# Kernel optimization log

Hardware: AMD Instinct MI355X
Metric: run time of the kernel (lower is better)

## Reference

```python
import jax, jax.numpy as jnp
import numpy as np

LRELU_SLOPE = 0.01  # torch nn.LeakyReLU default


def _lrelu(v):
    return jnp.where(v > 0, v, LRELU_SLOPE * v)


def setup_inputs() -> dict:
    key = jax.random.key(0)
    ks = jax.random.split(key, 9)
    B, C, T = 16, 1024, 1500
    nbins, hid, emb = 4096, 512, 256
    s = 0.02
    return {
        "feature": jax.random.normal(ks[0], (B, C, T), jnp.float32),
        "centroid": jax.random.normal(ks[1], (nbins, C), jnp.float32),
        "ew0": jax.random.normal(ks[2], (hid, C), jnp.float32) * s,
        "eb0": jnp.zeros((hid,), jnp.float32),
        "ew1": jax.random.normal(ks[3], (hid, hid), jnp.float32) * s,
        "eb1": jnp.zeros((hid,), jnp.float32),
        "ew2": jax.random.normal(ks[4], (emb, hid), jnp.float32) * s,
        "eb2": jnp.zeros((emb,), jnp.float32),
        "dw0": jax.random.normal(ks[5], (hid, emb), jnp.float32) * s,
        "db0": jnp.zeros((hid,), jnp.float32),
        "dw1": jax.random.normal(ks[6], (hid, hid), jnp.float32) * s,
        "db1": jnp.zeros((hid,), jnp.float32),
        "dw2": jax.random.normal(ks[7], (C, hid), jnp.float32) * s,
        "db2": jnp.zeros((C,), jnp.float32),
    }


def reference(feature, centroid, ew0, eb0, ew1, eb1, ew2, eb2,
              dw0, db0, dw1, db1, dw2, db2):
    B, C, T = feature.shape
    # --- nearest-centroid match: squared-norm expansion + matmul + argmin ---
    x = feature.transpose(0, 2, 1).reshape(-1, C)          # (B*T, C)
    c_norm = jnp.sum(centroid * centroid, axis=1)          # (nbins,)
    dist = (jnp.sum(x * x, axis=1, keepdims=True)
            - 2.0 * (x @ centroid.T)
            + c_norm[None, :])                             # (B*T, nbins)
    idx = jnp.argmin(dist, axis=1)                         # (B*T,)
    lin_dec = centroid[idx].reshape(B, T, C).transpose(0, 2, 1)  # (B, C, T)
    # --- speaker residual + refiner autoencoder (quantizer = identity) ---
    spk_raw = feature - lin_dec                            # (B, C, T)
    h = spk_raw.transpose(0, 2, 1)                         # (B, T, C)
    h = _lrelu(h @ ew0.T + eb0)
    h = _lrelu(h @ ew1.T + eb1)
    z = h @ ew2.T + eb2                                    # (B, T, emb)
    h = _lrelu(z @ dw0.T + db0)
    h = _lrelu(h @ dw1.T + db1)
    spk_dec = (h @ dw2.T + db2).transpose(0, 2, 1)         # (B, C, T)
    return lin_dec + spk_dec
```

## Files before the change

kernel.cpp:

```cpp
#include <hip/hip_runtime.h>


typedef unsigned short u16;
typedef unsigned int   u32;
typedef __bf16 bf16x8 __attribute__((ext_vector_type(8)));
typedef float  f32x4  __attribute__((ext_vector_type(4)));

#define AS1 __attribute__((address_space(1)))
#define AS3 __attribute__((address_space(3)))

__device__ __forceinline__ u16 rne_bf16(float f) {
  u32 u = __float_as_uint(f);
  u = (u + 0x7FFFu + ((u >> 16) & 1u)) >> 16;
  return (u16)u;
}
__device__ __forceinline__ float b2f(u16 h) {
  return __uint_as_float(((u32)h) << 16);
}


__global__ __launch_bounds__(256) void conv_centroid(
    const float* __restrict__ cent, u16* __restrict__ chi, u16* __restrict__ clo,
    float* __restrict__ cnorm, int K)
{
  int row  = blockIdx.x * 4 + (threadIdx.x >> 6);
  int lane = threadIdx.x & 63;
  const float* cr = cent + (size_t)row * K;
  float s = 0.f;
  for (int j = 0; j < K; j += 64) {
    int k = j + lane;
    float f = cr[k];
    s += f * f;
    u32 u = __float_as_uint(f);
    u32 hi = (u + 0x7FFFu + ((u >> 16) & 1u)) >> 16;
    float fhi = __uint_as_float(hi << 16);
    chi[(size_t)row * K + k] = (u16)hi;
    clo[(size_t)row * K + k] = rne_bf16(f - fhi);
  }
#pragma unroll
  for (int m = 1; m < 64; m <<= 1) s += __shfl_xor(s, m, 64);
  if (lane == 0) cnorm[row] = s;
}

__global__ __launch_bounds__(256) void conv_feature(
    const float* __restrict__ feat, u16* __restrict__ xhi, u16* __restrict__ xlo,
    int C, int T)
{
  __shared__ float tile[64][65];
  int bb = blockIdx.z, c0 = blockIdx.y * 64, t0 = blockIdx.x * 64;
  const float* fb = feat + (size_t)bb * C * T;
#pragma unroll
  for (int i = 0; i < 16; ++i) {
    int id = threadIdx.x + i * 256;
    int lc = id >> 6, lt = id & 63;
    int t = t0 + lt;
    tile[lc][lt] = (t < T) ? fb[(size_t)(c0 + lc) * T + t] : 0.f;
  }
  __syncthreads();
#pragma unroll
  for (int i = 0; i < 16; ++i) {
    int id = threadIdx.x + i * 256;
    int lt = id >> 6, lc = id & 63;
    int t = t0 + lt;
    if (t < T) {
      size_t row = (size_t)bb * T + t;
      float f = tile[lc][lt];
      u32 u = __float_as_uint(f);
      u32 hi = (u + 0x7FFFu + ((u >> 16) & 1u)) >> 16;
      float fhi = __uint_as_float(hi << 16);
      xhi[row * C + c0 + lc] = (u16)hi;
      xlo[row * C + c0 + lc] = rne_bf16(f - fhi);
    }
  }
}

__global__ __launch_bounds__(256) void f2bf(
    const float* __restrict__ s, u16* __restrict__ d, int n)
{
  int i = blockIdx.x * 256 + threadIdx.x;
  if (i < n) d[i] = rne_bf16(s[i]);
}


template<int KK, int NSEG>
__global__ __launch_bounds__(512, 2) void score256(
    const u16* __restrict__ A0, const u16* __restrict__ A1, const u16* __restrict__ A2,
    const u16* __restrict__ B0s, const u16* __restrict__ B1s, const u16* __restrict__ B2s,
    const float* __restrict__ cnb, float* __restrict__ pval, int* __restrict__ pidx,
    int M, int N)
{
  constexpr int NKTPS = KK / 64;
  constexpr int NKT   = NSEG * NKTPS;
  static_assert(NKT % 2 == 0, "even tile count");

  __shared__ f32x4 smem4[8192];
  char* smem = (char*)smem4;

  const int lane = threadIdx.x & 63;
  const int wid  = threadIdx.x >> 6;
  const int wr   = wid >> 2;
  const int wc   = wid & 3;

  const int rowBase = blockIdx.y * 256;
  const int colBase = blockIdx.x * 256;

  const int kswz  = ((lane & 7) ^ (lane >> 3)) << 4;
  const int kbase = (lane >> 4) << 4;

  const f32x4 zero4 = {0.f, 0.f, 0.f, 0.f};
  f32x4 acc[8][4];
#pragma unroll
  for (int i = 0; i < 8; ++i)
#pragma unroll
    for (int j = 0; j < 4; ++j) acc[i][j] = zero4;

  bf16x8 aR[4][2];
  bf16x8 bR[2][2][2];

  auto stageA = [&](int b, int h, int t) {
    int tc  = t < NKT ? t : NKT - 1;
    int seg = tc / NKTPS;
    int k0  = (tc - seg * NKTPS) << 6;
    const u16* S = (seg == 0 ? A0 : (seg == 1 ? A1 : A2));
    char* dst = smem + b * 32768 + h * 16384 + wid * 1024;
#pragma unroll
    for (int j = 0; j < 2; ++j) {
      int r  = h * 128 + j * 64 + wid * 8 + (lane >> 3);
      int gr = rowBase + r; gr = gr < M ? gr : M - 1;
      const char* ga = (const char*)S + ((size_t)gr * KK + k0) * 2 + kswz;
      __builtin_amdgcn_global_load_lds((const AS1 void*)ga,
                                       (AS3 void*)(dst + j * 8192), 16, 0, 0);
    }
  };
  auto stageB = [&](int b, int h, int t) {
    int tc  = t < NKT ? t : NKT - 1;
    int seg = tc / NKTPS;
    int k0  = (tc - seg * NKTPS) << 6;
    const u16* S = (seg == 0 ? B0s : (seg == 1 ? B1s : B2s));
    char* dst = smem + 65536 + b * 32768 + h * 16384 + wid * 1024;
#pragma unroll
    for (int j = 0; j < 2; ++j) {
      int r  = h * 128 + j * 64 + wid * 8 + (lane >> 3);
      int gr = colBase + r;
      const char* ga = (const char*)S + ((size_t)gr * KK + k0) * 2 + kswz;
      __builtin_amdgcn_global_load_lds((const AS1 void*)ga,
                                       (AS3 void*)(dst + j * 8192), 16, 0, 0);
    }
  };

#define LDA_Q(b, qm) do { \
  _Pragma("unroll") for (int mf = 0; mf < 4; ++mf) { \
    int row = wr * 128 + (qm) * 64 + mf * 16 + (lane & 15); \
    const char* p = smem + (b) * 32768 + row * 128; \
    int sw = (row & 7) << 4; \
    aR[mf][0] = *(const bf16x8*)(p + (kbase ^ sw)); \
    aR[mf][1] = *(const bf16x8*)(p + ((kbase + 64) ^ sw)); \
  } } while (0)

#define LDB_Q(b, qn) do { \
  _Pragma("unroll") for (int nf = 0; nf < 2; ++nf) { \
    int row = wc * 64 + (qn) * 32 + nf * 16 + (lane & 15); \
    const char* p = smem + 65536 + (b) * 32768 + row * 128; \
    int sw = (row & 7) << 4; \
    bR[qn][nf][0] = *(const bf16x8*)(p + (kbase ^ sw)); \
    bR[qn][nf][1] = *(const bf16x8*)(p + ((kbase + 64) ^ sw)); \
  } } while (0)

#define MMQ(qm, qn) do { \
  _Pragma("unroll") for (int mf = 0; mf < 4; ++mf) \
  _Pragma("unroll") for (int nf = 0; nf < 2; ++nf) { \
    acc[(qm)*4+mf][(qn)*2+nf] = __builtin_amdgcn_mfma_f32_16x16x32_bf16( \
        aR[mf][0], bR[qn][nf][0], acc[(qm)*4+mf][(qn)*2+nf], 0, 0, 0); \
    acc[(qm)*4+mf][(qn)*2+nf] = __builtin_amdgcn_mfma_f32_16x16x32_bf16( \
        aR[mf][1], bR[qn][nf][1], acc[(qm)*4+mf][(qn)*2+nf], 0, 0, 0); \
  } } while (0)

#define BAR()     __builtin_amdgcn_s_barrier()
#define PRIO1()   __builtin_amdgcn_s_setprio(1)
#define PRIO0()   __builtin_amdgcn_s_setprio(0)
#define VMCNT4()  asm volatile("s_waitcnt vmcnt(4)" ::: "memory")
#define LGKM8()   asm volatile("s_waitcnt lgkmcnt(8)" ::: "memory")
#define LGKM0_SB() do { asm volatile("s_waitcnt lgkmcnt(0)" ::: "memory"); \
                        __builtin_amdgcn_sched_barrier(0); } while (0)

  stageA(0, 0, 0); stageA(0, 1, 0); stageB(0, 0, 0); stageB(0, 1, 0);
  stageB(1, 0, 1); stageB(1, 1, 1);
  VMCNT4();
  BAR();

  for (int i = 0; i < NKT / 2; ++i) {
    const int t = 2 * i;
    LDA_Q(0, 0); LDB_Q(0, 0);
    stageA(1, 0, t + 1);
    LGKM8();
    BAR(); LGKM0_SB(); PRIO1(); MMQ(0, 0); PRIO0(); BAR();
    LDB_Q(0, 1);
    stageA(1, 1, t + 1);
    BAR(); LGKM0_SB(); PRIO1(); MMQ(0, 1); PRIO0(); BAR();
    LDA_Q(0, 1);
    stageB(0, 0, t + 2);
    BAR(); LGKM0_SB(); PRIO1(); MMQ(1, 1); PRIO0(); BAR();
    stageB(0, 1, t + 2);
    VMCNT4();
    BAR(); PRIO1(); MMQ(1, 0); PRIO0(); BAR();
    LDA_Q(1, 0); LDB_Q(1, 0);
    stageA(0, 0, t + 2);
    LGKM8();
    BAR(); LGKM0_SB(); PRIO1(); MMQ(0, 0); PRIO0(); BAR();
    LDB_Q(1, 1);
    stageA(0, 1, t + 2);
    BAR(); LGKM0_SB(); PRIO1(); MMQ(0, 1); PRIO0(); BAR();
    LDA_Q(1, 1);
    stageB(1, 0, t + 3);
    BAR(); LGKM0_SB(); PRIO1(); MMQ(1, 1); PRIO0(); BAR();
    stageB(1, 1, t + 3);
    VMCNT4();
    BAR(); PRIO1(); MMQ(1, 0); PRIO0(); BAR();
  }

  const int colL = colBase + wc * 64 + (lane & 15);
  float cn[4];
#pragma unroll
  for (int ni = 0; ni < 4; ++ni) cn[ni] = 0.5f * cnb[colL + ni * 16];
  const int nchunk = N >> 6;
  const int chunk  = (colBase >> 6) + wc;
#pragma unroll
  for (int mi = 0; mi < 8; ++mi) {
#pragma unroll
    for (int reg = 0; reg < 4; ++reg) {
      float best = acc[mi][0][reg] - cn[0];
      int   bc   = colL;
#pragma unroll
      for (int ni = 1; ni < 4; ++ni) {
        float v  = acc[mi][ni][reg] - cn[ni];
        int   c2 = colL + ni * 16;
        if (v > best || (v == best && c2 < bc)) { best = v; bc = c2; }
      }
#pragma unroll
      for (int m = 1; m < 16; m <<= 1) {
        float vo = __shfl_xor(best, m, 64);
        int   co = __shfl_xor(bc,   m, 64);
        if (vo > best || (vo == best && co < bc)) { best = vo; bc = co; }
      }
      if ((lane & 15) == 0) {
        int row = rowBase + wr * 128 + (mi >> 2) * 64 + (mi & 3) * 16
                + ((lane >> 4) << 2) + reg;
        if (row < M) {
          pval[(size_t)row * nchunk + chunk] = best;
          pidx[(size_t)row * nchunk + chunk] = bc;
        }
      }
    }
  }
#undef LDA_Q
#undef LDB_Q
#undef MMQ
#undef BAR
#undef PRIO1
#undef PRIO0
#undef VMCNT4
#undef LGKM8
#undef LGKM0_SB
}


template<int NSEG, bool SCORE, bool ACT>
__global__ __launch_bounds__(256) void gemm_bt(
    const u16* __restrict__ A0, const u16* __restrict__ A1, const u16* __restrict__ A2,
    const u16* __restrict__ B0, const u16* __restrict__ B1, const u16* __restrict__ B2,
    const float* __restrict__ cnb, u16* __restrict__ outb,
    float* __restrict__ pval, int* __restrict__ pidx,
    int M, int N, int K)
{
  __shared__ bf16x8 smem8[2048];
  char* smem = (char*)smem8;

  const int lane = threadIdx.x & 63;
  const int wid  = threadIdx.x >> 6;
  const int wm   = wid >> 1, wn = wid & 1;

  const int rowBase = blockIdx.y * 128;
  const int colBase = blockIdx.x * 128;

  const f32x4 zero4 = {0.f, 0.f, 0.f, 0.f};
  f32x4 acc[4][4];
#pragma unroll
  for (int i = 0; i < 4; ++i)
#pragma unroll
    for (int j = 0; j < 4; ++j) acc[i][j] = zero4;

  const int l8   = lane >> 3;
  const int kbsw = ((lane & 7) ^ l8) << 4;
  const int kseg = K >> 6;
  const int nkt  = NSEG * kseg;

  for (int kt = 0; kt < nkt; ++kt) {
    int seg, k0;
    if (NSEG == 1) { seg = 0; k0 = kt << 6; }
    else           { seg = kt / kseg; k0 = (kt - seg * kseg) << 6; }
    const u16* Aseg = (seg == 0) ? A0 : (seg == 1 ? A1 : A2);
    const u16* Bseg = (seg == 0) ? B0 : (seg == 1 ? B1 : B2);

#pragma unroll
    for (int i = 0; i < 4; ++i) {
      int c = wid * 4 + i;
      int r = c * 8 + l8;
      int gra = rowBase + r; gra = gra < M ? gra : (M - 1);
      const char* ga = (const char*)Aseg + ((size_t)gra * K + k0) * 2 + kbsw;
      __builtin_amdgcn_global_load_lds((const AS1 void*)ga,
                                       (AS3 void*)(smem + c * 1024), 16, 0, 0);
      int grb = colBase + r;
      const char* gb = (const char*)Bseg + ((size_t)grb * K + k0) * 2 + kbsw;
      __builtin_amdgcn_global_load_lds((const AS1 void*)gb,
                                       (AS3 void*)(smem + 16384 + c * 1024), 16, 0, 0);
    }
    __syncthreads();

#pragma unroll
    for (int kk = 0; kk < 64; kk += 32) {
      bf16x8 a[4], b[4];
      const int kb = (kk + ((lane >> 4) << 3)) << 1;
#pragma unroll
      for (int mf = 0; mf < 4; ++mf) {
        int row = wm * 64 + mf * 16 + (lane & 15);
        a[mf] = *(const bf16x8*)(smem + row * 128 + (kb ^ ((row & 7) << 4)));
      }
#pragma unroll
      for (int nf = 0; nf < 4; ++nf) {
        int row = wn * 64 + nf * 16 + (lane & 15);
        b[nf] = *(const bf16x8*)(smem + 16384 + row * 128 + (kb ^ ((row & 7) << 4)));
      }
#pragma unroll
      for (int mf = 0; mf < 4; ++mf)
#pragma unroll
        for (int nf = 0; nf < 4; ++nf)
          acc[mf][nf] = __builtin_amdgcn_mfma_f32_16x16x32_bf16(
              a[mf], b[nf], acc[mf][nf], 0, 0, 0);
    }
    __syncthreads();
  }

  const int colLane = colBase + wn * 64 + (lane & 15);

  if (SCORE) {
    float cn[4];
#pragma unroll
    for (int nf = 0; nf < 4; ++nf) cn[nf] = 0.5f * cnb[colLane + nf * 16];
    const int nchunk = N >> 6;
    const int chunk  = (colBase >> 6) + wn;
#pragma unroll
    for (int mf = 0; mf < 4; ++mf) {
#pragma unroll
      for (int reg = 0; reg < 4; ++reg) {
        float best = acc[mf][0][reg] - cn[0];
        int   bc   = colLane;
#pragma unroll
        for (int nf = 1; nf < 4; ++nf) {
          float v = acc[mf][nf][reg] - cn[nf];
          int c2 = colLane + nf * 16;
          if (v > best || (v == best && c2 < bc)) { best = v; bc = c2; }
        }
#pragma unroll
        for (int m = 1; m < 16; m <<= 1) {
          float vo = __shfl_xor(best, m, 64);
          int   co = __shfl_xor(bc,   m, 64);
          if (vo > best || (vo == best && co < bc)) { best = vo; bc = co; }
        }
        if ((lane & 15) == 0) {
          int row = rowBase + wm * 64 + mf * 16 + ((lane >> 4) << 2) + reg;
          if (row < M) {
            pval[(size_t)row * nchunk + chunk] = best;
            pidx[(size_t)row * nchunk + chunk] = bc;
          }
        }
      }
    }
  } else {
    float bl[4];
#pragma unroll
    for (int nf = 0; nf < 4; ++nf) bl[nf] = cnb[colLane + nf * 16];
#pragma unroll
    for (int mf = 0; mf < 4; ++mf)
#pragma unroll
      for (int nf = 0; nf < 4; ++nf)
#pragma unroll
        for (int reg = 0; reg < 4; ++reg) {
          int row = rowBase + wm * 64 + mf * 16 + ((lane >> 4) << 2) + reg;
          if (row < M) {
            float v = acc[mf][nf][reg] + bl[nf];
            if (ACT) v = v > 0.f ? v : 0.01f * v;
            outb[(size_t)row * N + colLane + nf * 16] = rne_bf16(v);
          }
        }
  }
}


__global__ __launch_bounds__(256) void argmax_reduce(
    const float* __restrict__ pval, const int* __restrict__ pidx,
    int* __restrict__ idxOut, int nchunk)
{
  int row  = blockIdx.x * 4 + (threadIdx.x >> 6);
  int lane = threadIdx.x & 63;
  float v = pval[(size_t)row * nchunk + lane];
  int   c = pidx[(size_t)row * nchunk + lane];
#pragma unroll
  for (int m = 1; m < 64; m <<= 1) {
    float vo = __shfl_xor(v, m, 64);
    int   co = __shfl_xor(c, m, 64);
    if (vo > v || (vo == v && co < c)) { v = vo; c = co; }
  }
  if (lane == 0) idxOut[row] = c;
}

__global__ __launch_bounds__(256) void build_spk(
    const u16* __restrict__ xhi, const u16* __restrict__ xlo,
    const float* __restrict__ cent, const int* __restrict__ idx,
    u16* __restrict__ spk, int C)
{
  int row = blockIdx.x;
  const float* cr = cent + (size_t)idx[row] * C;
  size_t base = (size_t)row * C;
  for (int c = threadIdx.x; c < C; c += 256) {
    float v = b2f(xhi[base + c]) + b2f(xlo[base + c]) - cr[c];
    spk[base + c] = rne_bf16(v);
  }
}

__global__ __launch_bounds__(256) void transpose_out(
    const u16* __restrict__ spkdec, const float* __restrict__ cent,
    const int* __restrict__ idx, float* __restrict__ out, int C, int T)
{
  __shared__ float tile[64][65];
  int r0 = blockIdx.x * 64, c0 = blockIdx.y * 64;
#pragma unroll
  for (int i = 0; i < 16; ++i) {
    int id = threadIdx.x + i * 256;
    int lr = id >> 6, lc = id & 63;
    int row = r0 + lr;
    tile[lr][lc] = b2f(spkdec[(size_t)row * C + c0 + lc])
                 + cent[(size_t)idx[row] * C + c0 + lc];
  }
  __syncthreads();
#pragma unroll
  for (int i = 0; i < 16; ++i) {
    int id = threadIdx.x + i * 256;
    int lc = id >> 6, lr = id & 63;
    int row = r0 + lr;
    int b = row / T, t = row - b * T;
    out[((size_t)b * C + c0 + lc) * T + t] = tile[lr][lc];
  }
}


extern "C" void kernel_launch(void* const* d_in, const int* in_sizes, int n_in,
                              void* d_out, int out_size, void* d_ws, size_t ws_size,
                              hipStream_t stream)
{
  const float* feature  = (const float*)d_in[0];
  const float* centroid = (const float*)d_in[1];
  const float* ew0 = (const float*)d_in[2];
  const float* eb0 = (const float*)d_in[3];
  const float* ew1 = (const float*)d_in[4];
  const float* eb1 = (const float*)d_in[5];
  const float* ew2 = (const float*)d_in[6];
  const float* eb2 = (const float*)d_in[7];
  const float* dw0 = (const float*)d_in[8];
  const float* db0 = (const float*)d_in[9];
  const float* dw1 = (const float*)d_in[10];
  const float* db1 = (const float*)d_in[11];
  const float* dw2 = (const float*)d_in[12];
  const float* db2 = (const float*)d_in[13];
  float* out = (float*)d_out;

  const int Bb = 16, C = 1024, T = 1500, M = Bb * T;
  const int NBIN = 4096, HID = 512, EMB = 256;
  const int MB  = (M + 127) / 128;
  const int MB2 = (M + 255) / 256;

  char* ws = (char*)d_ws;
  size_t off = 0;
  auto alloc = [&](size_t bytes) -> char* {
    char* p = ws + off;
    off += (bytes + 255) & ~(size_t)255;
    return p;
  };
  u16*   c_hi  = (u16*)  alloc((size_t)NBIN * C * 2);
  u16*   c_lo  = (u16*)  alloc((size_t)NBIN * C * 2);
  float* cnorm = (float*)alloc((size_t)NBIN * 4);
  u16*   wb0   = (u16*)  alloc((size_t)HID * C   * 2);
  u16*   wb1   = (u16*)  alloc((size_t)HID * HID * 2);
  u16*   wb2   = (u16*)  alloc((size_t)EMB * HID * 2);
  u16*   wb3   = (u16*)  alloc((size_t)HID * EMB * 2);
  u16*   wb4   = (u16*)  alloc((size_t)HID * HID * 2);
  u16*   wb5   = (u16*)  alloc((size_t)C   * HID * 2);
  u16*   x_hi  = (u16*)  alloc((size_t)M * C * 2);
  u16*   x_lo  = (u16*)  alloc((size_t)M * C * 2);
  int*   idx   = (int*)  alloc((size_t)M * 4);
  char*  spkR  =         alloc((size_t)M * C * 2);
  u16*   spk   = (u16*)spkR;
  float* pval  = (float*)spkR;
  int*   pidx  = (int*)(spkR + (size_t)M * 64 * 4);
  u16*   h1    = (u16*)  alloc((size_t)M * HID * 2);
  u16*   h2    = (u16*)  alloc((size_t)M * HID * 2);
  u16*   hz    = (u16*)  alloc((size_t)M * EMB * 2);

  conv_centroid<<<NBIN / 4, 256, 0, stream>>>(centroid, c_hi, c_lo, cnorm, C);
  conv_feature<<<dim3((T + 63) / 64, C / 64, Bb), 256, 0, stream>>>(feature, x_hi, x_lo, C, T);
  f2bf<<<(HID * C   + 255) / 256, 256, 0, stream>>>(ew0, wb0, HID * C);
  f2bf<<<(HID * HID + 255) / 256, 256, 0, stream>>>(ew1, wb1, HID * HID);
  f2bf<<<(EMB * HID + 255) / 256, 256, 0, stream>>>(ew2, wb2, EMB * HID);
  f2bf<<<(HID * EMB + 255) / 256, 256, 0, stream>>>(dw0, wb3, HID * EMB);
  f2bf<<<(HID * HID + 255) / 256, 256, 0, stream>>>(dw1, wb4, HID * HID);
  f2bf<<<(C   * HID + 255) / 256, 256, 0, stream>>>(dw2, wb5, C * HID);

  score256<1024, 3><<<dim3(NBIN / 256, MB2), 512, 0, stream>>>(
      x_hi, x_lo, x_hi, c_hi, c_hi, c_lo, cnorm, pval, pidx, M, NBIN);

  argmax_reduce<<<M / 4, 256, 0, stream>>>(pval, pidx, idx, NBIN / 64);
  build_spk<<<M, 256, 0, stream>>>(x_hi, x_lo, centroid, idx, spk, C);

  gemm_bt<1, false, true ><<<dim3(HID / 128, MB), 256, 0, stream>>>(
      spk, spk, spk, wb0, wb0, wb0, eb0, h1, nullptr, nullptr, M, HID, C);
  gemm_bt<1, false, true ><<<dim3(HID / 128, MB), 256, 0, stream>>>(
      h1, h1, h1, wb1, wb1, wb1, eb1, h2, nullptr, nullptr, M, HID, HID);
  gemm_bt<1, false, false><<<dim3(EMB / 128, MB), 256, 0, stream>>>(
      h2, h2, h2, wb2, wb2, wb2, eb2, hz, nullptr, nullptr, M, EMB, HID);
  gemm_bt<1, false, true ><<<dim3(HID / 128, MB), 256, 0, stream>>>(
      hz, hz, hz, wb3, wb3, wb3, db0, h1, nullptr, nullptr, M, HID, EMB);
  gemm_bt<1, false, true ><<<dim3(HID / 128, MB), 256, 0, stream>>>(
      h1, h1, h1, wb4, wb4, wb4, db1, h2, nullptr, nullptr, M, HID, HID);
  gemm_bt<1, false, false><<<dim3(C / 128, MB), 256, 0, stream>>>(
      h2, h2, h2, wb5, wb5, wb5, db2, spk, nullptr, nullptr, M, C, HID);

  transpose_out<<<dim3(M / 64, C / 64), 256, 0, stream>>>(spk, centroid, idx, out, C, T);
}
```

Before: 1.016 ms.

## Replace three-pass split-bf16 centroid scoring with bf16 pass plus candidate rescan

```diff
diff --git a/kernel.cpp b/kernel.cpp
--- a/kernel.cpp
+++ b/kernel.cpp
@@ -8,6 +8,8 @@
 
 #define AS1 __attribute__((address_space(1)))
 #define AS3 __attribute__((address_space(3)))
+
+#define LIST_CAP 2048
 
 __device__ __forceinline__ u16 rne_bf16(float f) {
   u32 u = __float_as_uint(f);
@@ -264,61 +266,88 @@
 }
 
 
-template<int NSEG, bool SCORE, bool ACT>
-__global__ __launch_bounds__(256) void gemm_bt(
-    const u16* __restrict__ A0, const u16* __restrict__ A1, const u16* __restrict__ A2,
-    const u16* __restrict__ B0, const u16* __restrict__ B1, const u16* __restrict__ B2,
-    const float* __restrict__ cnb, u16* __restrict__ outb,
-    float* __restrict__ pval, int* __restrict__ pidx,
-    int M, int N, int K)
-{
-  __shared__ bf16x8 smem8[2048];
-  char* smem = (char*)smem8;
-
-  const int lane = threadIdx.x & 63;
-  const int wid  = threadIdx.x >> 6;
+__global__ __launch_bounds__(256) void cand_select(
+    const float* __restrict__ pval1, int* __restrict__ lists,
+    int* __restrict__ cnt)
+{
+  int row  = blockIdx.x * 4 + (threadIdx.x >> 6);
+  int lane = threadIdx.x & 63;
+  float v = pval1[(size_t)row * 64 + lane];
+  float m = v;
+#pragma unroll
+  for (int s = 1; s < 64; s <<= 1) m = fmaxf(m, __shfl_xor(m, s, 64));
+  if (v >= m - 1.0f) {
+    int pos = atomicAdd(&cnt[lane], 1);
+    if (pos < LIST_CAP) lists[lane * LIST_CAP + pos] = row;
+  }
+}
+
+
+template<int KK>
+__global__ __launch_bounds__(256) void rescan(
+    const u16* __restrict__ xhi, const u16* __restrict__ xlo,
+    const u16* __restrict__ chi, const u16* __restrict__ clo,
+    const float* __restrict__ cnorm,
+    const int* __restrict__ lists, const int* __restrict__ cnt,
+    float* __restrict__ pval2, int* __restrict__ pidx2)
+{
+  __shared__ char  smem[24576];
+  __shared__ int   rlist[128];
+  __shared__ float sval[128];
+  __shared__ int   sidx[128];
+
+  const int chunk = blockIdx.x;
+  const int n     = cnt[chunk];
+  const int m0    = blockIdx.y * 128;
+  if (m0 >= n) return;
+
+  const int tid  = threadIdx.x;
+  const int lane = tid & 63;
+  const int wid  = tid >> 6;
   const int wm   = wid >> 1, wn = wid & 1;
 
-  const int rowBase = blockIdx.y * 128;
-  const int colBase = blockIdx.x * 128;
+  if (tid < 128) {
+    int m = m0 + tid;
+    rlist[tid] = lists[chunk * LIST_CAP + (m < n ? m : n - 1)];
+  }
+  __syncthreads();
+
+  const int kswz = ((lane & 7) ^ (lane >> 3)) << 4;
+  size_t aoff[4];
+#pragma unroll
+  for (int j = 0; j < 4; ++j) {
+    int r = (wid * 4 + j) * 8 + (lane >> 3);
+    aoff[j] = (size_t)rlist[r] * KK * 2 + kswz;
+  }
+  size_t boff[2];
+#pragma unroll
+  for (int j = 0; j < 2; ++j) {
+    int r = (wid * 2 + j) * 8 + (lane >> 3);
+    boff[j] = (size_t)(chunk * 64 + r) * KK * 2 + kswz;
+  }
 
   const f32x4 zero4 = {0.f, 0.f, 0.f, 0.f};
-  f32x4 acc[4][4];
-#pragma unroll
-  for (int i = 0; i < 4; ++i)
-#pragma unroll
-    for (int j = 0; j < 4; ++j) acc[i][j] = zero4;
-
-  const int l8   = lane >> 3;
-  const int kbsw = ((lane & 7) ^ l8) << 4;
-  const int kseg = K >> 6;
-  const int nkt  = NSEG * kseg;
-
-  for (int kt = 0; kt < nkt; ++kt) {
-    int seg, k0;
-    if (NSEG == 1) { seg = 0; k0 = kt << 6; }
-    else           { seg = kt / kseg; k0 = (kt - seg * kseg) << 6; }
-    const u16* Aseg = (seg == 0) ? A0 : (seg == 1 ? A1 : A2);
-    const u16* Bseg = (seg == 0) ? B0 : (seg == 1 ? B1 : B2);
-
-#pragma unroll
-    for (int i = 0; i < 4; ++i) {
-      int c = wid * 4 + i;
-      int r = c * 8 + l8;
-      int gra = rowBase + r; gra = gra < M ? gra : (M - 1);
-      const char* ga = (const char*)Aseg + ((size_t)gra * K + k0) * 2 + kbsw;
-      __builtin_amdgcn_global_load_lds((const AS1 void*)ga,
-                                       (AS3 void*)(smem + c * 1024), 16, 0, 0);
-      int grb = colBase + r;
-      const char* gb = (const char*)Bseg + ((size_t)grb * K + k0) * 2 + kbsw;
-      __builtin_amdgcn_global_load_lds((const AS1 void*)gb,
-                                       (AS3 void*)(smem + 16384 + c * 1024), 16, 0, 0);
-    }
+  f32x4 acc[4][2];
+#pragma unroll
+  for (int i = 0; i < 4; ++i) { acc[i][0] = zero4; acc[i][1] = zero4; }
+
+  for (int kt = 0; kt < 3 * (KK / 64); ++kt) {
+    int seg = kt / (KK / 64);
+    int k0b = (kt % (KK / 64)) << 7;
+    const char* Asrc = (const char*)(seg == 1 ? xlo : xhi) + k0b;
+    const char* Bsrc = (const char*)(seg == 2 ? clo : chi) + k0b;
+#pragma unroll
+    for (int j = 0; j < 4; ++j)
+      __builtin_amdgcn_global_load_lds((const AS1 void*)(Asrc + aoff[j]),
+          (AS3 void*)(smem + (wid * 4 + j) * 1024), 16, 0, 0);
+#pragma unroll
+    for (int j = 0; j < 2; ++j)
+      __builtin_amdgcn_global_load_lds((const AS1 void*)(Bsrc + boff[j]),
+          (AS3 void*)(smem + 16384 + (wid * 2 + j) * 1024), 16, 0, 0);
     __syncthreads();
-
 #pragma unroll
     for (int kk = 0; kk < 64; kk += 32) {
-      bf16x8 a[4], b[4];
+      bf16x8 a[4], b[2];
       const int kb = (kk + ((lane >> 4) << 3)) << 1;
 #pragma unroll
       for (int mf = 0; mf < 4; ++mf) {
@@ -326,72 +355,63 @@
         a[mf] = *(const bf16x8*)(smem + row * 128 + (kb ^ ((row & 7) << 4)));
       }
 #pragma unroll
-      for (int nf = 0; nf < 4; ++nf) {
-        int row = wn * 64 + nf * 16 + (lane & 15);
+      for (int nf = 0; nf < 2; ++nf) {
+        int row = wn * 32 + nf * 16 + (lane & 15);
         b[nf] = *(const bf16x8*)(smem + 16384 + row * 128 + (kb ^ ((row & 7) << 4)));
       }
 #pragma unroll
       for (int mf = 0; mf < 4; ++mf)
 #pragma unroll
-        for (int nf = 0; nf < 4; ++nf)
+        for (int nf = 0; nf < 2; ++nf)
           acc[mf][nf] = __builtin_amdgcn_mfma_f32_16x16x32_bf16(
               a[mf], b[nf], acc[mf][nf], 0, 0, 0);
     }
     __syncthreads();
   }
 
-  const int colLane = colBase + wn * 64 + (lane & 15);
-
-  if (SCORE) {
-    float cn[4];
-#pragma unroll
-    for (int nf = 0; nf < 4; ++nf) cn[nf] = 0.5f * cnb[colLane + nf * 16];
-    const int nchunk = N >> 6;
-    const int chunk  = (colBase >> 6) + wn;
-#pragma unroll
-    for (int mf = 0; mf < 4; ++mf) {
+  const int colL = chunk * 64 + wn * 32 + (lane & 15);
+  const float cn0 = 0.5f * cnorm[colL];
+  const float cn1 = 0.5f * cnorm[colL + 16];
+  float rbest[4][4]; int rbc[4][4];
+#pragma unroll
+  for (int mf = 0; mf < 4; ++mf)
+#pragma unroll
+    for (int reg = 0; reg < 4; ++reg) {
+      float best = acc[mf][0][reg] - cn0;
+      int   bc   = colL;
+      float v1   = acc[mf][1][reg] - cn1;
+      if (v1 > best || (v1 == best && colL + 16 < bc)) { best = v1; bc = colL + 16; }
+#pragma unroll
+      for (int m = 1; m < 16; m <<= 1) {
+        float vo = __shfl_xor(best, m, 64);
+        int   co = __shfl_xor(bc,   m, 64);
+        if (vo > best || (vo == best && co < bc)) { best = vo; bc = co; }
+      }
+      rbest[mf][reg] = best; rbc[mf][reg] = bc;
+    }
+  if (wn == 1 && (lane & 15) == 0) {
+#pragma unroll
+    for (int mf = 0; mf < 4; ++mf)
 #pragma unroll
       for (int reg = 0; reg < 4; ++reg) {
-        float best = acc[mf][0][reg] - cn[0];
-        int   bc   = colLane;
-#pragma unroll
-        for (int nf = 1; nf < 4; ++nf) {
-          float v = acc[mf][nf][reg] - cn[nf];
-          int c2 = colLane + nf * 16;
-          if (v > best || (v == best && c2 < bc)) { best = v; bc = c2; }
-        }
-#pragma unroll
-        for (int m = 1; m < 16; m <<= 1) {
-          float vo = __shfl_xor(best, m, 64);
-          int   co = __shfl_xor(bc,   m, 64);
-          if (vo > best || (vo == best && co < bc)) { best = vo; bc = co; }
-        }
-        if ((lane & 15) == 0) {
-          int row = rowBase + wm * 64 + mf * 16 + ((lane >> 4) << 2) + reg;
-          if (row < M) {
-            pval[(size_t)row * nchunk + chunk] = best;
-            pidx[(size_t)row * nchunk + chunk] = bc;
-          }
-        }
-      }
-    }
-  } else {
-    float bl[4];
-#pragma unroll
-    for (int nf = 0; nf < 4; ++nf) bl[nf] = cnb[colLane + nf * 16];
+        int rloc = wm * 64 + mf * 16 + ((lane >> 4) << 2) + reg;
+        sval[rloc] = rbest[mf][reg]; sidx[rloc] = rbc[mf][reg];
+      }
+  }
+  __syncthreads();
+  if (wn == 0 && (lane & 15) == 0) {
 #pragma unroll
     for (int mf = 0; mf < 4; ++mf)
 #pragma unroll
-      for (int nf = 0; nf < 4; ++nf)
-#pragma unroll
-        for (int reg = 0; reg < 4; ++reg) {
-          int row = rowBase + wm * 64 + mf * 16 + ((lane >> 4) << 2) + reg;
-          if (row < M) {
-            float v = acc[mf][nf][reg] + bl[nf];
-            if (ACT) v = v > 0.f ? v : 0.01f * v;
-            outb[(size_t)row * N + colLane + nf * 16] = rne_bf16(v);
-          }
-        }
+      for (int reg = 0; reg < 4; ++reg) {
+        int rloc = wm * 64 + mf * 16 + ((lane >> 4) << 2) + reg;
+        float best = rbest[mf][reg]; int bc = rbc[mf][reg];
+        float vo = sval[rloc]; int co = sidx[rloc];
+        if (vo > best || (vo == best && co < bc)) { best = vo; bc = co; }
+        int row = rlist[rloc];
+        pval2[(size_t)row * 64 + chunk] = best;
+        pidx2[(size_t)row * 64 + chunk] = bc;
+      }
   }
 }
 
@@ -450,6 +470,95 @@
     int b = row / T, t = row - b * T;
     out[((size_t)b * C + c0 + lc) * T + t] = tile[lr][lc];
   }
+}
+
+
+template<int NSEG, bool ACT>
+__global__ __launch_bounds__(256) void gemm_bt(
+    const u16* __restrict__ A0,
+    const u16* __restrict__ B0,
+    const float* __restrict__ cnb, u16* __restrict__ outb,
+    int M, int N, int K)
+{
+  __shared__ bf16x8 smem8[2048];
+  char* smem = (char*)smem8;
+
+  const int lane = threadIdx.x & 63;
+  const int wid  = threadIdx.x >> 6;
+  const int wm   = wid >> 1, wn = wid & 1;
+
+  const int rowBase = blockIdx.y * 128;
+  const int colBase = blockIdx.x * 128;
+
+  const f32x4 zero4 = {0.f, 0.f, 0.f, 0.f};
+  f32x4 acc[4][4];
+#pragma unroll
+  for (int i = 0; i < 4; ++i)
+#pragma unroll
+    for (int j = 0; j < 4; ++j) acc[i][j] = zero4;
+
+  const int l8   = lane >> 3;
+  const int kbsw = ((lane & 7) ^ l8) << 4;
+  const int nkt  = K >> 6;
+
+  for (int kt = 0; kt < nkt; ++kt) {
+    int k0 = kt << 6;
+#pragma unroll
+    for (int i = 0; i < 4; ++i) {
+      int c = wid * 4 + i;
+      int r = c * 8 + l8;
+      int gra = rowBase + r; gra = gra < M ? gra : (M - 1);
+      const char* ga = (const char*)A0 + ((size_t)gra * K + k0) * 2 + kbsw;
+      __builtin_amdgcn_global_load_lds((const AS1 void*)ga,
+                                       (AS3 void*)(smem + c * 1024), 16, 0, 0);
+      int grb = colBase + r;
+      const char* gb = (const char*)B0 + ((size_t)grb * K + k0) * 2 + kbsw;
+      __builtin_amdgcn_global_load_lds((const AS1 void*)gb,
+                                       (AS3 void*)(smem + 16384 + c * 1024), 16, 0, 0);
+    }
+    __syncthreads();
+
+#pragma unroll
+    for (int kk = 0; kk < 64; kk += 32) {
+      bf16x8 a[4], b[4];
+      const int kb = (kk + ((lane >> 4) << 3)) << 1;
+#pragma unroll
+      for (int mf = 0; mf < 4; ++mf) {
+        int row = wm * 64 + mf * 16 + (lane & 15);
+        a[mf] = *(const bf16x8*)(smem + row * 128 + (kb ^ ((row & 7) << 4)));
+      }
+#pragma unroll
+      for (int nf = 0; nf < 4; ++nf) {
+        int row = wn * 64 + nf * 16 + (lane & 15);
+        b[nf] = *(const bf16x8*)(smem + 16384 + row * 128 + (kb ^ ((row & 7) << 4)));
+      }
+#pragma unroll
+      for (int mf = 0; mf < 4; ++mf)
+#pragma unroll
+        for (int nf = 0; nf < 4; ++nf)
+          acc[mf][nf] = __builtin_amdgcn_mfma_f32_16x16x32_bf16(
+              a[mf], b[nf], acc[mf][nf], 0, 0, 0);
+    }
+    __syncthreads();
+  }
+
+  const int colLane = colBase + wn * 64 + (lane & 15);
+  float bl[4];
+#pragma unroll
+  for (int nf = 0; nf < 4; ++nf) bl[nf] = cnb[colLane + nf * 16];
+#pragma unroll
+  for (int mf = 0; mf < 4; ++mf)
+#pragma unroll
+    for (int nf = 0; nf < 4; ++nf)
+#pragma unroll
+      for (int reg = 0; reg < 4; ++reg) {
+        int row = rowBase + wm * 64 + mf * 16 + ((lane >> 4) << 2) + reg;
+        if (row < M) {
+          float v = acc[mf][nf][reg] + bl[nf];
+          if (ACT) v = v > 0.f ? v : 0.01f * v;
+          outb[(size_t)row * N + colLane + nf * 16] = rne_bf16(v);
+        }
+      }
 }
 
 
@@ -499,11 +608,15 @@
   int*   idx   = (int*)  alloc((size_t)M * 4);
   char*  spkR  =         alloc((size_t)M * C * 2);
   u16*   spk   = (u16*)spkR;
-  float* pval  = (float*)spkR;
-  int*   pidx  = (int*)(spkR + (size_t)M * 64 * 4);
+  float* pval1 = (float*)spkR;
+  int*   pidx1 = (int*)(spkR + (size_t)M * 64 * 4);
   u16*   h1    = (u16*)  alloc((size_t)M * HID * 2);
   u16*   h2    = (u16*)  alloc((size_t)M * HID * 2);
   u16*   hz    = (u16*)  alloc((size_t)M * EMB * 2);
+  float* pval2 = (float*)h1;
+  int*   pidx2 = (int*)h2;
+  int*   lists = (int*)hz;
+  int*   cnt   = (int*)(hz + (size_t)64 * LIST_CAP * 2);
 
   conv_centroid<<<NBIN / 4, 256, 0, stream>>>(centroid, c_hi, c_lo, cnorm, C);
   conv_feature<<<dim3((T + 63) / 64, C / 64, Bb), 256, 0, stream>>>(feature, x_hi, x_lo, C, T);
@@ -514,24 +627,25 @@
   f2bf<<<(HID * HID + 255) / 256, 256, 0, stream>>>(dw1, wb4, HID * HID);
   f2bf<<<(C   * HID + 255) / 256, 256, 0, stream>>>(dw2, wb5, C * HID);
 
-  score256<1024, 3><<<dim3(NBIN / 256, MB2), 512, 0, stream>>>(
-      x_hi, x_lo, x_hi, c_hi, c_hi, c_lo, cnorm, pval, pidx, M, NBIN);
-
-  argmax_reduce<<<M / 4, 256, 0, stream>>>(pval, pidx, idx, NBIN / 64);
+  hipMemsetAsync(cnt, 0, 64 * sizeof(int), stream);
+  hipMemsetAsync(pval2, 0xFE, (size_t)M * 64 * 4, stream);
+
+  score256<1024, 1><<<dim3(NBIN / 256, MB2), 512, 0, stream>>>(
+      x_hi, x_hi, x_hi, c_hi, c_hi, c_hi, cnorm, pval1, pidx1, M, NBIN);
+
+  cand_select<<<M / 4, 256, 0, stream>>>(pval1, lists, cnt);
+  rescan<1024><<<dim3(64, LIST_CAP / 128), 256, 0, stream>>>(
+      x_hi, x_lo, c_hi, c_lo, cnorm, lists, cnt, pval2, pidx2);
+  argmax_reduce<<<M / 4, 256, 0, stream>>>(pval2, pidx2, idx, 64);
+
   build_spk<<<M, 256, 0, stream>>>(x_hi, x_lo, centroid, idx, spk, C);
 
-  gemm_bt<1, false, true ><<<dim3(HID / 128, MB), 256, 0, stream>>>(
-      spk, spk, spk, wb0, wb0, wb0, eb0, h1, nullptr, nullptr, M, HID, C);
-  gemm_bt<1, false, true ><<<dim3(HID / 128, MB), 256, 0, stream>>>(
-      h1, h1, h1, wb1, wb1, wb1, eb1, h2, nullptr, nullptr, M, HID, HID);
-  gemm_bt<1, false, false><<<dim3(EMB / 128, MB), 256, 0, stream>>>(
-      h2, h2, h2, wb2, wb2, wb2, eb2, hz, nullptr, nullptr, M, EMB, HID);
-  gemm_bt<1, false, true ><<<dim3(HID / 128, MB), 256, 0, stream>>>(
-      hz, hz, hz, wb3, wb3, wb3, db0, h1, nullptr, nullptr, M, HID, EMB);
-  gemm_bt<1, false, true ><<<dim3(HID / 128, MB), 256, 0, stream>>>(
-      h1, h1, h1, wb4, wb4, wb4, db1, h2, nullptr, nullptr, M, HID, HID);
-  gemm_bt<1, false, false><<<dim3(C / 128, MB), 256, 0, stream>>>(
-      h2, h2, h2, wb5, wb5, wb5, db2, spk, nullptr, nullptr, M, C, HID);
+  gemm_bt<1, true ><<<dim3(HID / 128, MB), 256, 0, stream>>>(spk, wb0, eb0, h1, M, HID, C);
+  gemm_bt<1, true ><<<dim3(HID / 128, MB), 256, 0, stream>>>(h1, wb1, eb1, h2, M, HID, HID);
+  gemm_bt<1, false><<<dim3(EMB / 128, MB), 256, 0, stream>>>(h2, wb2, eb2, (u16*)hz, M, EMB, HID);
+  gemm_bt<1, true ><<<dim3(HID / 128, MB), 256, 0, stream>>>((u16*)hz, wb3, db0, h1, M, HID, EMB);
+  gemm_bt<1, true ><<<dim3(HID / 128, MB), 256, 0, stream>>>(h1, wb4, db1, h2, M, HID, HID);
+  gemm_bt<1, false><<<dim3(C / 128, MB), 256, 0, stream>>>(h2, wb5, db2, spk, M, C, HID);
 
   transpose_out<<<dim3(M / 64, C / 64), 256, 0, stream>>>(spk, centroid, idx, out, C, T);
 }
```

New measurement: 943.9 us. -7.1%, faster.
